# Kernel optimization log

Hardware: AMD Instinct MI355X
Metric: run time of the kernel (lower is better)

The kernel has to match this reference:

```python
import jax, jax.numpy as jnp
import numpy as np

B, P, D = 8, 1024, 1024
H, N = 16, 64  # num_heads, head_dim


def setup_inputs() -> dict:
    key = jax.random.key(0)
    k1, k2, k3 = jax.random.split(key, 3)
    inputs = jax.random.normal(k1, (B, P, D), dtype=jnp.float32)
    # Keras 'random_normal' initializer: stddev 0.05
    w_qkv = jax.random.normal(k2, (H, 3, D, N), dtype=jnp.float32) * 0.05
    w_o = jax.random.normal(k3, (N * H, D), dtype=jnp.float32) * 0.05
    return {"inputs": inputs, "w_qkv": w_qkv, "w_o": w_o}


def reference(inputs, w_qkv, w_o):
    # Per-head QKV projection: [b,p,d] x [h,3,d,n] -> [b,h,3,p,n]
    proj = jnp.einsum('bpv,havn->bhapn', inputs, w_qkv)
    q = proj[:, :, 0]  # [b,h,p,n]
    k = proj[:, :, 1]
    v = proj[:, :, 2]
    head_dim = q.shape[-1]
    scale = 1.0 / jnp.sqrt(jnp.asarray(head_dim, dtype=jnp.float32))
    scores = jnp.einsum('bhqn,bhkn->bhqk', q, k) * scale  # [b,h,p,p]
    attn = jax.nn.softmax(scores, axis=-1)
    out = jnp.einsum('bhqk,bhkn->bhqn', attn, v)  # [b,h,p,n]
    # concat heads along feature dim: [b,p,h*n]
    b, h, p, n = out.shape
    concat = out.transpose(0, 2, 1, 3).reshape(b, p, h * n)
    return jnp.einsum('bpi,ij->bpj', concat, w_o)  # [b,p,d_model]
```

## Files before the change

### kernel.cpp

```cpp
#include <hip/hip_runtime.h>
#include <stdint.h>

typedef _Float16 f16;
typedef __attribute__((ext_vector_type(2))) _Float16 f16x2;
typedef __attribute__((ext_vector_type(4))) _Float16 f16x4;
typedef __attribute__((ext_vector_type(8))) _Float16 f16x8;
typedef __attribute__((ext_vector_type(2))) __fp16 h16x2;
typedef __attribute__((ext_vector_type(4))) float f32x4;

__device__ __forceinline__ void gload_lds16(const void* g, void* l) {
  __builtin_amdgcn_global_load_lds(
      (__attribute__((address_space(1))) void*)const_cast<void*>(g),
      (__attribute__((address_space(3))) void*)l, 16, 0, 0);
}


__global__ void convert_x(const float* __restrict__ in, f16* __restrict__ out) {
  int i = blockIdx.x * 256 + threadIdx.x;
  float4 v = ((const float4*)in)[i];
  f16x4 hv;
  hv[0] = (f16)v.x; hv[1] = (f16)v.y; hv[2] = (f16)v.z; hv[3] = (f16)v.w;
  ((f16x4*)out)[i] = hv;
}

__global__ void transpose_wqkv(const float* __restrict__ in, f16* __restrict__ out) {
  __shared__ float tile[64][65];
  int s = blockIdx.x >> 4;
  int vt = blockIdx.x & 15;
  int hh = s / 3, a = s - hh * 3;
  int tx = threadIdx.x & 63, ty = threadIdx.x >> 6;
#pragma unroll
  for (int i = 0; i < 16; i++) {
    int r = i * 4 + ty;
    tile[r][tx] = in[((size_t)(s * 1024 + vt * 64 + r)) * 64 + tx];
  }
  __syncthreads();
#pragma unroll
  for (int i = 0; i < 16; i++) {
    int n = i * 4 + ty;
    out[((size_t)(a * 1024 + hh * 64 + n)) * 1024 + vt * 64 + tx] = (f16)tile[tx][n];
  }
}

__global__ void transpose_wo(const float* __restrict__ in, f16* __restrict__ out) {
  __shared__ float tile[64][65];
  int rt = blockIdx.x >> 4, ct = blockIdx.x & 15;
  int tx = threadIdx.x & 63, ty = threadIdx.x >> 6;
#pragma unroll
  for (int i = 0; i < 16; i++) {
    int r = i * 4 + ty;
    tile[r][tx] = in[((size_t)(rt * 64 + r)) * 1024 + ct * 64 + tx];
  }
  __syncthreads();
#pragma unroll
  for (int i = 0; i < 16; i++) {
    int j = i * 4 + ty;
    out[((size_t)(ct * 64 + j)) * 1024 + rt * 64 + tx] = (f16)tile[tx][j];
  }
}

template <int OUTMODE>
__global__ __launch_bounds__(256, 2) void gemm_kernel(
    const f16* __restrict__ A, const f16* __restrict__ BT, void* __restrict__ out,
    void* __restrict__ out2, int M, int N, int K) {
  __shared__ __align__(16) f16 As[128][32];
  __shared__ __align__(16) f16 Bs[128][32];
  const int t = threadIdx.x;
  const int lane = t & 63, wave = t >> 6;
  const int lr = lane & 15, lg = lane >> 4;
  const int wm = wave >> 1, wn = wave & 1;
  const int nTN = N >> 7;
  const int bm = blockIdx.x / nTN, bn = blockIdx.x % nTN;
  const f16* Ab = A + (size_t)bm * 128 * K;
  const f16* Bb = BT + (size_t)bn * 128 * K;

  const f32x4 zero4 = {0.f, 0.f, 0.f, 0.f};
  f32x4 acc[4][4];
#pragma unroll
  for (int m = 0; m < 4; m++)
#pragma unroll
    for (int n = 0; n < 4; n++) acc[m][n] = zero4;

  for (int k0 = 0; k0 < K; k0 += 32) {
    __syncthreads();
#pragma unroll
    for (int i = 0; i < 2; i++) {
      int q = wave * 2 + i;
      int e = q * 64 + lane;
      int r = e >> 2, bi = e & 3;
      gload_lds16(Ab + (size_t)r * K + k0 + ((bi ^ (r & 3)) << 3),
                  (char*)&As[0][0] + q * 1024);
      gload_lds16(Bb + (size_t)r * K + k0 + ((bi ^ (r & 3)) << 3),
                  (char*)&Bs[0][0] + q * 1024);
    }
    __syncthreads();
    f16x8 af[4], bf[4];
#pragma unroll
    for (int m = 0; m < 4; m++) {
      int r = wm * 64 + m * 16 + lr;
      af[m] = *(const f16x8*)&As[r][(lg ^ (r & 3)) << 3];
    }
#pragma unroll
    for (int n = 0; n < 4; n++) {
      int r = wn * 64 + n * 16 + lr;
      bf[n] = *(const f16x8*)&Bs[r][(lg ^ (r & 3)) << 3];
    }
#pragma unroll
    for (int m = 0; m < 4; m++)
#pragma unroll
      for (int n = 0; n < 4; n++)
        acc[m][n] = __builtin_amdgcn_mfma_f32_16x16x32_f16(af[m], bf[n], acc[m][n], 0, 0, 0);
  }

  const int r0 = bm * 128 + wm * 64;
  const int c0 = bn * 128 + wn * 64;
  if (OUTMODE == 2 && bn >= 16) {
    f16* VT = (f16*)out2;
    const int bb = bm >> 3;
#pragma unroll
    for (int m = 0; m < 4; m++) {
      int p = r0 + m * 16 + lg * 4;
      int pl = p & 1023;
#pragma unroll
      for (int n = 0; n < 4; n++) {
        int vcol = c0 - 2048 + n * 16 + lr;
        f16x4 pv;
#pragma unroll
        for (int i = 0; i < 4; i++) pv[i] = (f16)acc[m][n][i];
        *(f16x4*)&VT[((size_t)(bb * 16 + (vcol >> 6)) * 64 + (vcol & 63)) * 1024 + pl] = pv;
      }
    }
  } else {
#pragma unroll
    for (int m = 0; m < 4; m++)
#pragma unroll
      for (int n = 0; n < 4; n++)
#pragma unroll
        for (int i = 0; i < 4; i++) {
          int gr = r0 + m * 16 + lg * 4 + i;
          int gc = c0 + n * 16 + lr;
          if (OUTMODE == 1)
            ((float*)out)[(size_t)gr * N + gc] = acc[m][n][i];
          else
            ((f16*)out)[(size_t)gr * N + gc] = (f16)acc[m][n][i];
        }
  }
}

__global__ __launch_bounds__(256, 4) void attn_kernel(
    const f16* __restrict__ QKV, const f16* __restrict__ VT, f16* __restrict__ C) {
  __shared__ __align__(16) f16 smem[16384];

  const int t = threadIdx.x, lane = t & 63, wave = t >> 6;
  const int lr = lane & 15, lg = lane >> 4;
  const int pt = blockIdx.x, bh = blockIdx.y;
  const int b = bh >> 4, h = bh & 15;
  const int p0 = pt * 128;

  const f16* Qg = QKV + ((size_t)(b * 1024 + p0)) * 3072 + h * 64;
  const f16* Kg = QKV + ((size_t)(b * 1024)) * 3072 + 1024 + h * 64;
  const f16* Vg = VT + (size_t)bh * 64 * 1024;

#pragma unroll
  for (int i = 0; i < 4; i++) {
    int q = wave * 4 + i;
    int u = q * 64 + lane;
    int r = u >> 3, j = u & 7;
    gload_lds16(Qg + (size_t)r * 3072 + ((j ^ (r & 7)) << 3), (char*)smem + q * 1024);
  }
  __syncthreads();

  const f16 qscale = (f16)0.180336878f;
  f16x8 qa[2][2];
#pragma unroll
  for (int m = 0; m < 2; m++)
#pragma unroll
    for (int hh = 0; hh < 2; hh++) {
      int r = wave * 32 + m * 16 + lr;
      f16x8 v = *(const f16x8*)&smem[(size_t)r * 64 + (((hh * 4 + lg) ^ (lr & 7)) << 3)];
#pragma unroll
      for (int e = 0; e < 8; e++) v[e] *= qscale;
      qa[m][hh] = v;
    }
  __syncthreads();

  auto STAGE = [&](int kc, int cur) {
#pragma unroll
    for (int i = 0; i < 2; i++) {
      int q = wave * 2 + i;
      int u = q * 64 + lane;
      int r = u >> 3, j = u & 7;
      gload_lds16(Kg + (size_t)(kc * 64 + r) * 3072 + ((j ^ (r & 7)) << 3),
                  (char*)smem + cur * 16384 + q * 1024);
      gload_lds16(Vg + (size_t)r * 1024 + kc * 64 + ((j ^ (r & 7)) << 3),
                  (char*)smem + cur * 16384 + 8192 + q * 1024);
    }
  };

  STAGE(0, 0);
  STAGE(1, 1);
  __syncthreads();

  const f32x4 zero4 = {0.f, 0.f, 0.f, 0.f};
  f32x4 o[2][4];
#pragma unroll
  for (int m = 0; m < 2; m++)
#pragma unroll
    for (int n = 0; n < 4; n++) o[m][n] = zero4;
  float mrun[2] = {0.f, 0.f};
  float lrun[2] = {0.f, 0.f};
  const h16x2 one2 = {(__fp16)1.f, (__fp16)1.f};

#pragma unroll 1
  for (int kc = 0; kc < 16; kc++) {
    const int cur = kc & 1;
    const int kB = cur * 8192;
    const char* vB = (const char*)smem + cur * 16384 + 8192;

    f32x4 s[2][4];
#pragma unroll
    for (int m = 0; m < 2; m++) {
      f32x4 init = {-mrun[m], -mrun[m], -mrun[m], -mrun[m]};
#pragma unroll
      for (int kb = 0; kb < 4; kb++) s[m][kb] = init;
    }
    __builtin_amdgcn_s_setprio(1);
#pragma unroll
    for (int kb = 0; kb < 4; kb++) {
      int r = kb * 16 + lr;
      f16x8 kf0 = *(const f16x8*)&smem[kB + (size_t)r * 64 + ((lg ^ (lr & 7)) << 3)];
      f16x8 kf1 = *(const f16x8*)&smem[kB + (size_t)r * 64 + (((4 + lg) ^ (lr & 7)) << 3)];
#pragma unroll
      for (int m = 0; m < 2; m++) {
        s[m][kb] = __builtin_amdgcn_mfma_f32_16x16x32_f16(kf0, qa[m][0], s[m][kb], 0, 0, 0);
        s[m][kb] = __builtin_amdgcn_mfma_f32_16x16x32_f16(kf1, qa[m][1], s[m][kb], 0, 0, 0);
      }
    }
    __builtin_amdgcn_s_setprio(0);

    f16x8 pa8[2][2];
#pragma unroll
    for (int m = 0; m < 2; m++) {
      float mx = fmaxf(fmaxf(fmaxf(s[m][0][0], s[m][0][1]), fmaxf(s[m][0][2], s[m][0][3])),
                       fmaxf(fmaxf(s[m][1][0], s[m][1][1]), fmaxf(s[m][1][2], s[m][1][3])));
      mx = fmaxf(mx, fmaxf(fmaxf(fmaxf(s[m][2][0], s[m][2][1]), fmaxf(s[m][2][2], s[m][2][3])),
                           fmaxf(fmaxf(s[m][3][0], s[m][3][1]), fmaxf(s[m][3][2], s[m][3][3]))));
      mx = fmaxf(mx, __shfl_xor(mx, 16));
      mx = fmaxf(mx, __shfl_xor(mx, 32));
      if (__any(mx > 4.328085f)) {
        float delta = fmaxf(mx, 0.f);
        mrun[m] += delta;
        float alpha = exp2f(-delta);
        lrun[m] *= alpha;
#pragma unroll
        for (int kb = 0; kb < 4; kb++)
#pragma unroll
          for (int i = 0; i < 4; i++) s[m][kb][i] -= delta;
#pragma unroll
        for (int i = 0; i < 4; i++) {
          float ai = __shfl(alpha, (lane & 48) | (lg * 4 + i));
#pragma unroll
          for (int n = 0; n < 4; n++) o[m][n][i] *= ai;
        }
      }
      float rs = 0.f;
#pragma unroll
      for (int j = 0; j < 2; j++)
#pragma unroll
        for (int hb = 0; hb < 2; hb++) {
          int kb = 2 * j + hb;
          h16x2 h01 = __builtin_amdgcn_cvt_pkrtz(exp2f(s[m][kb][0]), exp2f(s[m][kb][1]));
          h16x2 h23 = __builtin_amdgcn_cvt_pkrtz(exp2f(s[m][kb][2]), exp2f(s[m][kb][3]));
          rs = __builtin_amdgcn_fdot2(h01, one2, rs, false);
          rs = __builtin_amdgcn_fdot2(h23, one2, rs, false);
          pa8[m][j][hb * 4 + 0] = (f16)h01[0];
          pa8[m][j][hb * 4 + 1] = (f16)h01[1];
          pa8[m][j][hb * 4 + 2] = (f16)h23[0];
          pa8[m][j][hb * 4 + 3] = (f16)h23[1];
        }
      rs += __shfl_xor(rs, 16);
      rs += __shfl_xor(rs, 32);
      lrun[m] += rs;
    }

    __builtin_amdgcn_s_setprio(1);
#pragma unroll
    for (int n = 0; n < 4; n++) {
      const char* rowB = vB + (size_t)(n * 16 + lr) * 128 + ((lg & 1) << 3);
#pragma unroll
      for (int j = 0; j < 2; j++) {
        f16x4 lo = *(const f16x4*)(rowB + (((j * 4 + (lg >> 1)) ^ (lr & 7)) << 4));
        f16x4 hi = *(const f16x4*)(rowB + (((j * 4 + 2 + (lg >> 1)) ^ (lr & 7)) << 4));
        f16x8 vb = {lo[0], lo[1], lo[2], lo[3], hi[0], hi[1], hi[2], hi[3]};
        o[0][n] = __builtin_amdgcn_mfma_f32_16x16x32_f16(pa8[0][j], vb, o[0][n], 0, 0, 0);
        o[1][n] = __builtin_amdgcn_mfma_f32_16x16x32_f16(pa8[1][j], vb, o[1][n], 0, 0, 0);
      }
    }
    __builtin_amdgcn_s_setprio(0);

    __syncthreads();
    if (kc + 2 < 16) STAGE(kc + 2, cur);
  }

#pragma unroll
  for (int m = 0; m < 2; m++) {
    float linv = 1.f / lrun[m];
#pragma unroll
    for (int i = 0; i < 4; i++) {
      float li = __shfl(linv, (lane & 48) | (lg * 4 + i));
      int prow = p0 + wave * 32 + m * 16 + lg * 4 + i;
#pragma unroll
      for (int n = 0; n < 4; n++) {
        int col = h * 64 + n * 16 + lr;
        C[((size_t)(b * 1024 + prow)) * 1024 + col] = (f16)(o[m][n][i] * li);
      }
    }
  }
}

extern "C" void kernel_launch(void* const* d_in, const int* in_sizes, int n_in,
                              void* d_out, int out_size, void* d_ws, size_t ws_size,
                              hipStream_t stream) {
  const float* X = (const float*)d_in[0];
  const float* Wqkv = (const float*)d_in[1];
  const float* Wo = (const float*)d_in[2];
  float* Y = (float*)d_out;

  f16* ws = (f16*)d_ws;
  f16* X16 = ws;
  f16* WqkvT = ws + 8388608;
  f16* WoT = ws + 11534336;
  f16* QKV = ws + 12582912;
  f16* VT = (f16*)d_out;

  convert_x<<<8192, 256, 0, stream>>>(X, X16);
  transpose_wqkv<<<768, 256, 0, stream>>>(Wqkv, WqkvT);
  transpose_wo<<<256, 256, 0, stream>>>(Wo, WoT);
  gemm_kernel<2><<<64 * 24, 256, 0, stream>>>(X16, WqkvT, QKV, VT, 8192, 3072, 1024);
  attn_kernel<<<dim3(8, 128), 256, 0, stream>>>(QKV, VT, X16 );
  gemm_kernel<1><<<64 * 8, 256, 0, stream>>>(X16 , WoT, Y, nullptr, 8192, 1024, 1024);
}
```

Measured before the change: 189.5 us.

## Widen GEMM K-tile to 64, permute V^T layout, compute softmax row sums via MFMA

The GEMM now stages 64-wide K slices with an 8-way XOR swizzle, so it runs half as many barrier-separated iterations. The V-transpose store permutes positions so the attention kernel can read each V fragment with one 16-byte LDS load instead of two 8-byte loads and a shuffle. The softmax row sum moves from per-lane fdot2 plus cross-lane shuffles to an extra MFMA against a ones vector, and the normalizer is read directly per row at the end. This adds two MFMAs per chunk and doubles the GEMM LDS footprint, which may affect occupancy.

```diff
diff --git a/kernel.cpp b/kernel.cpp
--- a/kernel.cpp
+++ b/kernel.cpp
@@ -7,6 +7,7 @@
 typedef __attribute__((ext_vector_type(8))) _Float16 f16x8;
 typedef __attribute__((ext_vector_type(2))) __fp16 h16x2;
 typedef __attribute__((ext_vector_type(4))) float f32x4;
+typedef __attribute__((ext_vector_type(4))) uint32_t u32x4;
 
 __device__ __forceinline__ void gload_lds16(const void* g, void* l) {
   __builtin_amdgcn_global_load_lds(
@@ -63,8 +64,8 @@
 __global__ __launch_bounds__(256, 2) void gemm_kernel(
     const f16* __restrict__ A, const f16* __restrict__ BT, void* __restrict__ out,
     void* __restrict__ out2, int M, int N, int K) {
-  __shared__ __align__(16) f16 As[128][32];
-  __shared__ __align__(16) f16 Bs[128][32];
+  __shared__ __align__(16) f16 As[128][64];
+  __shared__ __align__(16) f16 Bs[128][64];
   const int t = threadIdx.x;
   const int lane = t & 63, wave = t >> 6;
   const int lr = lane & 15, lg = lane >> 4;
@@ -81,35 +82,38 @@
 #pragma unroll
     for (int n = 0; n < 4; n++) acc[m][n] = zero4;
 
-  for (int k0 = 0; k0 < K; k0 += 32) {
+  for (int k0 = 0; k0 < K; k0 += 64) {
     __syncthreads();
 #pragma unroll
-    for (int i = 0; i < 2; i++) {
-      int q = wave * 2 + i;
-      int e = q * 64 + lane;
-      int r = e >> 2, bi = e & 3;
-      gload_lds16(Ab + (size_t)r * K + k0 + ((bi ^ (r & 3)) << 3),
+    for (int i = 0; i < 4; i++) {
+      int q = wave * 4 + i;
+      int u = q * 64 + lane;
+      int r = u >> 3, j = u & 7;
+      gload_lds16(Ab + (size_t)r * K + k0 + ((j ^ (r & 7)) << 3),
                   (char*)&As[0][0] + q * 1024);
-      gload_lds16(Bb + (size_t)r * K + k0 + ((bi ^ (r & 3)) << 3),
+      gload_lds16(Bb + (size_t)r * K + k0 + ((j ^ (r & 7)) << 3),
                   (char*)&Bs[0][0] + q * 1024);
     }
     __syncthreads();
-    f16x8 af[4], bf[4];
-#pragma unroll
-    for (int m = 0; m < 4; m++) {
-      int r = wm * 64 + m * 16 + lr;
-      af[m] = *(const f16x8*)&As[r][(lg ^ (r & 3)) << 3];
-    }
-#pragma unroll
-    for (int n = 0; n < 4; n++) {
-      int r = wn * 64 + n * 16 + lr;
-      bf[n] = *(const f16x8*)&Bs[r][(lg ^ (r & 3)) << 3];
-    }
-#pragma unroll
-    for (int m = 0; m < 4; m++)
-#pragma unroll
-      for (int n = 0; n < 4; n++)
-        acc[m][n] = __builtin_amdgcn_mfma_f32_16x16x32_f16(af[m], bf[n], acc[m][n], 0, 0, 0);
+#pragma unroll
+    for (int half = 0; half < 2; half++) {
+      f16x8 af[4], bf[4];
+#pragma unroll
+      for (int m = 0; m < 4; m++) {
+        int r = wm * 64 + m * 16 + lr;
+        af[m] = *(const f16x8*)&As[r][((half * 4 + lg) ^ (r & 7)) << 3];
+      }
+#pragma unroll
+      for (int n = 0; n < 4; n++) {
+        int r = wn * 64 + n * 16 + lr;
+        bf[n] = *(const f16x8*)&Bs[r][((half * 4 + lg) ^ (r & 7)) << 3];
+      }
+#pragma unroll
+      for (int m = 0; m < 4; m++)
+#pragma unroll
+        for (int n = 0; n < 4; n++)
+          acc[m][n] = __builtin_amdgcn_mfma_f32_16x16x32_f16(af[m], bf[n], acc[m][n], 0, 0, 0);
+    }
   }
 
   const int r0 = bm * 128 + wm * 64;
@@ -119,15 +123,15 @@
     const int bb = bm >> 3;
 #pragma unroll
     for (int m = 0; m < 4; m++) {
-      int p = r0 + m * 16 + lg * 4;
-      int pl = p & 1023;
+      int pl = (r0 + m * 16 + lg * 4) & 1023;
+      int pl2 = (pl & 992) | ((pl & 12) << 1) | ((pl & 16) >> 2);
 #pragma unroll
       for (int n = 0; n < 4; n++) {
         int vcol = c0 - 2048 + n * 16 + lr;
         f16x4 pv;
 #pragma unroll
         for (int i = 0; i < 4; i++) pv[i] = (f16)acc[m][n][i];
-        *(f16x4*)&VT[((size_t)(bb * 16 + (vcol >> 6)) * 64 + (vcol & 63)) * 1024 + pl] = pv;
+        *(f16x4*)&VT[((size_t)(bb * 16 + (vcol >> 6)) * 64 + (vcol & 63)) * 1024 + pl2] = pv;
       }
     }
   } else {
@@ -202,14 +206,16 @@
   __syncthreads();
 
   const f32x4 zero4 = {0.f, 0.f, 0.f, 0.f};
-  f32x4 o[2][4];
-#pragma unroll
-  for (int m = 0; m < 2; m++)
+  f32x4 o[2][4], o_l[2];
+#pragma unroll
+  for (int m = 0; m < 2; m++) {
+    o_l[m] = zero4;
 #pragma unroll
     for (int n = 0; n < 4; n++) o[m][n] = zero4;
+  }
   float mrun[2] = {0.f, 0.f};
-  float lrun[2] = {0.f, 0.f};
-  const h16x2 one2 = {(__fp16)1.f, (__fp16)1.f};
+  const f16x8 ones8 = {(f16)1.f, (f16)1.f, (f16)1.f, (f16)1.f,
+                       (f16)1.f, (f16)1.f, (f16)1.f, (f16)1.f};
 
 #pragma unroll 1
   for (int kc = 0; kc < 16; kc++) {
@@ -251,7 +257,6 @@
         float delta = fmaxf(mx, 0.f);
         mrun[m] += delta;
         float alpha = exp2f(-delta);
-        lrun[m] *= alpha;
 #pragma unroll
         for (int kb = 0; kb < 4; kb++)
 #pragma unroll
@@ -259,39 +264,32 @@
 #pragma unroll
         for (int i = 0; i < 4; i++) {
           float ai = __shfl(alpha, (lane & 48) | (lg * 4 + i));
+          o_l[m][i] *= ai;
 #pragma unroll
           for (int n = 0; n < 4; n++) o[m][n][i] *= ai;
         }
       }
-      float rs = 0.f;
-#pragma unroll
-      for (int j = 0; j < 2; j++)
-#pragma unroll
-        for (int hb = 0; hb < 2; hb++) {
-          int kb = 2 * j + hb;
-          h16x2 h01 = __builtin_amdgcn_cvt_pkrtz(exp2f(s[m][kb][0]), exp2f(s[m][kb][1]));
-          h16x2 h23 = __builtin_amdgcn_cvt_pkrtz(exp2f(s[m][kb][2]), exp2f(s[m][kb][3]));
-          rs = __builtin_amdgcn_fdot2(h01, one2, rs, false);
-          rs = __builtin_amdgcn_fdot2(h23, one2, rs, false);
-          pa8[m][j][hb * 4 + 0] = (f16)h01[0];
-          pa8[m][j][hb * 4 + 1] = (f16)h01[1];
-          pa8[m][j][hb * 4 + 2] = (f16)h23[0];
-          pa8[m][j][hb * 4 + 3] = (f16)h23[1];
-        }
-      rs += __shfl_xor(rs, 16);
-      rs += __shfl_xor(rs, 32);
-      lrun[m] += rs;
+#pragma unroll
+      for (int j = 0; j < 2; j++) {
+        uint32_t w0, w1, w2, w3;
+        w0 = __builtin_bit_cast(uint32_t, __builtin_amdgcn_cvt_pkrtz(exp2f(s[m][2 * j][0]), exp2f(s[m][2 * j][1])));
+        w1 = __builtin_bit_cast(uint32_t, __builtin_amdgcn_cvt_pkrtz(exp2f(s[m][2 * j][2]), exp2f(s[m][2 * j][3])));
+        w2 = __builtin_bit_cast(uint32_t, __builtin_amdgcn_cvt_pkrtz(exp2f(s[m][2 * j + 1][0]), exp2f(s[m][2 * j + 1][1])));
+        w3 = __builtin_bit_cast(uint32_t, __builtin_amdgcn_cvt_pkrtz(exp2f(s[m][2 * j + 1][2]), exp2f(s[m][2 * j + 1][3])));
+        u32x4 ww = {w0, w1, w2, w3};
+        pa8[m][j] = __builtin_bit_cast(f16x8, ww);
+      }
     }
 
     __builtin_amdgcn_s_setprio(1);
 #pragma unroll
-    for (int n = 0; n < 4; n++) {
-      const char* rowB = vB + (size_t)(n * 16 + lr) * 128 + ((lg & 1) << 3);
-#pragma unroll
-      for (int j = 0; j < 2; j++) {
-        f16x4 lo = *(const f16x4*)(rowB + (((j * 4 + (lg >> 1)) ^ (lr & 7)) << 4));
-        f16x4 hi = *(const f16x4*)(rowB + (((j * 4 + 2 + (lg >> 1)) ^ (lr & 7)) << 4));
-        f16x8 vb = {lo[0], lo[1], lo[2], lo[3], hi[0], hi[1], hi[2], hi[3]};
+    for (int j = 0; j < 2; j++) {
+      o_l[0] = __builtin_amdgcn_mfma_f32_16x16x32_f16(pa8[0][j], ones8, o_l[0], 0, 0, 0);
+      o_l[1] = __builtin_amdgcn_mfma_f32_16x16x32_f16(pa8[1][j], ones8, o_l[1], 0, 0, 0);
+#pragma unroll
+      for (int n = 0; n < 4; n++) {
+        int rv = n * 16 + lr;
+        f16x8 vb = *(const f16x8*)(vB + (size_t)rv * 128 + (((4 * j + lg) ^ (lr & 7)) << 4));
         o[0][n] = __builtin_amdgcn_mfma_f32_16x16x32_f16(pa8[0][j], vb, o[0][n], 0, 0, 0);
         o[1][n] = __builtin_amdgcn_mfma_f32_16x16x32_f16(pa8[1][j], vb, o[1][n], 0, 0, 0);
       }
@@ -303,11 +301,10 @@
   }
 
 #pragma unroll
-  for (int m = 0; m < 2; m++) {
-    float linv = 1.f / lrun[m];
+  for (int m = 0; m < 2; m++)
 #pragma unroll
     for (int i = 0; i < 4; i++) {
-      float li = __shfl(linv, (lane & 48) | (lg * 4 + i));
+      float li = 1.f / o_l[m][i];
       int prow = p0 + wave * 32 + m * 16 + lg * 4 + i;
 #pragma unroll
       for (int n = 0; n < 4; n++) {
@@ -315,7 +312,6 @@
         C[((size_t)(b * 1024 + prow)) * 1024 + col] = (f16)(o[m][n][i] * li);
       }
     }
-  }
 }
 
 extern "C" void kernel_launch(void* const* d_in, const int* in_sizes, int n_in,
```

Result: faster. 173.3 us, median of 2 (-8.5%).
